# Kernel tuning notes

Measured on AMD Instinct MI355X. Metric: run time of the kernel, lower is better.

The kernel has to match this reference:

```python
import jax, jax.numpy as jnp
import numpy as np

N_USERS = 100000
N_ITEMS = 50000
D = 64
L = 3          # TopKformer_layers
E = 1000000    # number of train (user,item) edges


def setup_inputs() -> dict:
    key = jax.random.key(0)
    k1, k2, k3, k4, k5 = jax.random.split(key, 5)
    return {
        "users_w": jax.random.normal(k1, (N_USERS, D), jnp.float32) * 0.1,
        "items_w": jax.random.normal(k2, (N_ITEMS, D), jnp.float32) * 0.1,
        "beta_w": jax.random.normal(k3, (N_USERS, L), jnp.float32),
        "train_user": jax.random.randint(k4, (E,), 0, N_USERS, dtype=jnp.int32),
        "train_item": jax.random.randint(k5, (E,), 0, N_ITEMS, dtype=jnp.int32),
    }


def reference(users_w, items_w, beta_w, train_user, train_item):
    """Model.computer(): LightGCN-style bipartite propagation where each
    layer's user update is gated by a learned per-user beta = tanh(beta_w).
    Returns concat([user_embs, item_embs]) after L propagation layers."""
    beta = jnp.tanh(beta_w)  # [N_USERS, L], as in Model.beta_value

    # symmetric degree normalization 1/sqrt(d_u * d_i) over train edges
    ones = jnp.ones(train_user.shape[0], users_w.dtype)
    du = jnp.clip(jax.ops.segment_sum(ones, train_user, N_USERS), 1.0)
    di = jnp.clip(jax.ops.segment_sum(ones, train_item, N_ITEMS), 1.0)
    norm = (1.0 / jnp.sqrt(du[train_user] * di[train_item]))[:, None]  # [E,1]

    u_emb, i_emb = users_w, items_w
    for l in range(L):
        # gather neighbor embeddings along edges, scatter-add back (irregular access)
        msg_u = jax.ops.segment_sum(i_emb[train_item] * norm, train_user, N_USERS)
        msg_i = jax.ops.segment_sum(u_emb[train_user] * norm, train_item, N_ITEMS)
        u_emb = msg_u + beta[:, l:l + 1] * u_emb  # beta-weighted residual (per user)
        i_emb = msg_i
    return jnp.concatenate([u_emb, i_emb], axis=0)  # [N_USERS+N_ITEMS, D]
```

## Files before the change

### kernel.cpp

```cpp
#include <hip/hip_runtime.h>

#define NUSERS 100000
#define NITEMS 50000
#define NV (NUSERS + NITEMS)
#define DIM 64
#define NLAYERS 3
#define PAD 64
#define BINSHIFT 9
#define BINSZ 512
#define NBINS ((NV + BINSZ - 1) / BINSZ)
#define EPB 1024

typedef _Float16 half4v __attribute__((ext_vector_type(4)));
typedef _Float16 half8v __attribute__((ext_vector_type(8)));

__global__ void hist_kernel(const int* __restrict__ tu, const int* __restrict__ ti,
                            int* __restrict__ cnt, int E) {
    __shared__ int h[NBINS];
    int t = threadIdx.x, b = blockIdx.x;
    for (int i = t; i < NBINS; i += 256) h[i] = 0;
    __syncthreads();
    int base = b * EPB;
#pragma unroll
    for (int j = 0; j < 4; ++j) {
        int e = base + t + 256 * j;
        if (e < E) {
            atomicAdd(&h[tu[e] >> BINSHIFT], 1);
            atomicAdd(&h[(NUSERS + ti[e]) >> BINSHIFT], 1);
        }
    }
    __syncthreads();
    for (int i = t; i < NBINS; i += 256) cnt[(size_t)b * NBINS + i] = h[i];
}

__global__ void colscan_kernel(int* __restrict__ cnt, int* __restrict__ bintot, int nblk) {
    __shared__ int sh[256];
    int bin = blockIdx.x, t = threadIdx.x;
    int chunk = (nblk + 255) / 256;
    int v[8];
    int sum = 0;
    for (int j = 0; j < chunk; ++j) {
        int blk = t * chunk + j;
        v[j] = (blk < nblk) ? cnt[(size_t)blk * NBINS + bin] : 0;
        sum += v[j];
    }
    sh[t] = sum;
    __syncthreads();
    for (int d = 1; d < 256; d <<= 1) {
        int x = (t >= d) ? sh[t - d] : 0;
        __syncthreads();
        sh[t] += x;
        __syncthreads();
    }
    int run = sh[t] - sum;
    for (int j = 0; j < chunk; ++j) {
        int blk = t * chunk + j;
        if (blk < nblk) { cnt[(size_t)blk * NBINS + bin] = run; run += v[j]; }
    }
    if (t == 255) bintot[bin] = sh[255];
}

__global__ void binscan_kernel(const int* __restrict__ bintot, int* __restrict__ binstart) {
    __shared__ int sh[512];
    int t = threadIdx.x;
    int v = (t < NBINS) ? bintot[t] : 0;
    sh[t] = v;
    __syncthreads();
    for (int d = 1; d < 512; d <<= 1) {
        int x = (t >= d) ? sh[t - d] : 0;
        __syncthreads();
        sh[t] += x;
        __syncthreads();
    }
    if (t < NBINS) binstart[t] = sh[t] - v;
    if (t == NBINS - 1) binstart[NBINS] = sh[t];
}

__global__ void scatter_kernel(const int* __restrict__ tu, const int* __restrict__ ti,
                               const int* __restrict__ cnt, const int* __restrict__ binstart,
                               unsigned int* __restrict__ binbuf, int E) {
    __shared__ int h[NBINS];
    __shared__ int bb[NBINS];
    __shared__ int bs[NBINS];
    int t = threadIdx.x, b = blockIdx.x;
    for (int i = t; i < NBINS; i += 256) {
        h[i] = 0;
        bb[i] = cnt[(size_t)b * NBINS + i];
        bs[i] = binstart[i];
    }
    __syncthreads();
    int base = b * EPB;
#pragma unroll
    for (int j = 0; j < 4; ++j) {
        int e = base + t + 256 * j;
        if (e < E) {
            int u = tu[e];
            int w = NUSERS + ti[e];
            int bu = u >> BINSHIFT, bw = w >> BINSHIFT;
            int r1 = atomicAdd(&h[bu], 1);
            int r2 = atomicAdd(&h[bw], 1);
            binbuf[bs[bu] + bb[bu] + r1] = ((unsigned)(u & (BINSZ - 1)) << 18) | (unsigned)w;
            binbuf[bs[bw] + bb[bw] + r2] = ((unsigned)(w & (BINSZ - 1)) << 18) | (unsigned)u;
        }
    }
}

__global__ void bfill_kernel(const unsigned int* __restrict__ binbuf,
                             const int* __restrict__ binstart,
                             int* __restrict__ deg, int* __restrict__ adj) {
    __shared__ int c[BINSZ];
    int bin = blockIdx.x, t = threadIdx.x;
    c[t] = 0;
    __syncthreads();
    int start = binstart[bin];
    int n = binstart[bin + 1] - start;
    int vbase = bin << BINSHIFT;
    for (int k = t; k < n; k += 512) {
        unsigned rec = binbuf[start + k];
        int vloc = rec >> 18;
        int nbr = (int)(rec & 0x3FFFFu);
        int r = atomicAdd(&c[vloc], 1);
        adj[((vbase + vloc) << 6) + r] = nbr << 7;
    }
    __syncthreads();
    int v = vbase + t;
    if (v < NV) deg[v] = c[t];
}

__global__ void init_kernel(const float* __restrict__ users_w, const float* __restrict__ items_w,
                            const int* __restrict__ deg, _Float16* __restrict__ Yh,
                            _Float16* __restrict__ Dh) {
    int t = blockIdx.x * blockDim.x + threadIdx.x;
    int n4 = NV * (DIM / 4);
    if (t >= n4) {
        int z = t - n4;
        if (z < 16) reinterpret_cast<half4v*>(Yh + (size_t)NV * DIM)[z] = half4v{};
        else if (z < 32) reinterpret_cast<half4v*>(Dh + (size_t)NV * DIM)[z - 16] = half4v{};
        return;
    }
    int v = t >> 4;
    float r = rsqrtf(fmaxf((float)deg[v], 1.0f));
    const float4* src = (v < NUSERS)
        ? reinterpret_cast<const float4*>(users_w) + t
        : reinterpret_cast<const float4*>(items_w) + (t - NUSERS * (DIM / 4));
    float4 x = *src;
    half4v h;
    h.x = (_Float16)(x.x * r);
    h.y = (_Float16)(x.y * r);
    h.z = (_Float16)(x.z * r);
    h.w = (_Float16)(x.w * r);
    reinterpret_cast<half4v*>(Yh)[t] = h;
}

template <bool FINAL>
__global__ void gather_kernel(const _Float16* __restrict__ Yh, const int* __restrict__ deg,
                              const int* __restrict__ adj,
                              const float* __restrict__ beta_w,
                              void* __restrict__ dst_v, int layer) {
    int wid = (blockIdx.x * blockDim.x + threadIdx.x) >> 6;
    int lane = threadIdx.x & 63;
    if (wid >= NV) return;
    int g = lane >> 3;
    int p = lane & 7;
    int s = wid << 6;
    const char* rowb = (const char*)Yh + p * 16;
    const int NVS = NV << 7;

    int dg = deg[wid];
    int raw0 = adj[s + g];
    int raw1 = adj[s + 8 + g];
    int raw2 = adj[s + 16 + g];
    int raw3 = adj[s + 24 + g];
    bool isU = wid < NUSERS;
    float bw_ = 0.f;
    half8v hy = {};
    if (isU && g == 0) {
        bw_ = beta_w[wid * NLAYERS + layer];
        hy = *reinterpret_cast<const half8v*>(Yh + (size_t)wid * DIM + p * 8);
    }

    int o0 = (g      < dg) ? raw0 : NVS;
    int o1 = (8 + g  < dg) ? raw1 : NVS;
    half8v h0 = *reinterpret_cast<const half8v*>(rowb + (size_t)(unsigned)o0);
    half8v h1 = *reinterpret_cast<const half8v*>(rowb + (size_t)(unsigned)o1);

    half8v hs;
    if (dg > 16) {
        int o2 = (16 + g < dg) ? raw2 : NVS;
        int o3 = (24 + g < dg) ? raw3 : NVS;
        half8v h2 = *reinterpret_cast<const half8v*>(rowb + (size_t)(unsigned)o2);
        half8v h3 = *reinterpret_cast<const half8v*>(rowb + (size_t)(unsigned)o3);
        hs = (h0 + h1) + (h2 + h3);
    } else {
        hs = h0 + h1;
    }
    float a[8];
#pragma unroll
    for (int j = 0; j < 8; ++j) a[j] = (float)hs[j];

    if (dg > 32) {
#pragma unroll
        for (int jb = 0; jb < 4; ++jb) {
            int slotbase = 32 + jb * 8;
            if (slotbase < dg) {
                int ks = slotbase + g;
                int rw = adj[s + ks];
                int oj = (ks < dg) ? rw : NVS;
                half8v hj = *reinterpret_cast<const half8v*>(rowb + (size_t)(unsigned)oj);
#pragma unroll
                for (int j = 0; j < 8; ++j) a[j] += (float)hj[j];
            }
        }
    }

#pragma unroll
    for (int j = 0; j < 8; ++j) a[j] += __shfl_xor(a[j], 8);
#pragma unroll
    for (int j = 0; j < 8; ++j) a[j] += __shfl_xor(a[j], 16);
#pragma unroll
    for (int j = 0; j < 8; ++j) a[j] += __shfl_xor(a[j], 32);

    if (g == 0) {
        float fdg = fmaxf((float)dg, 1.0f);
        float r = rsqrtf(fdg);
        float b = isU ? tanhf(bw_) : 0.f;
        if (!FINAL) {
            float rr = r * r;
            half8v o;
#pragma unroll
            for (int j = 0; j < 8; ++j) o[j] = (_Float16)(rr * a[j] + b * (float)hy[j]);
            reinterpret_cast<half8v*>((_Float16*)dst_v + (size_t)wid * DIM)[p] = o;
        } else {
            float c = b * __builtin_sqrtf(fdg);
            float4 o0f, o1f;
            o0f.x = r * a[0] + c * (float)hy[0];
            o0f.y = r * a[1] + c * (float)hy[1];
            o0f.z = r * a[2] + c * (float)hy[2];
            o0f.w = r * a[3] + c * (float)hy[3];
            o1f.x = r * a[4] + c * (float)hy[4];
            o1f.y = r * a[5] + c * (float)hy[5];
            o1f.z = r * a[6] + c * (float)hy[6];
            o1f.w = r * a[7] + c * (float)hy[7];
            float4* dp = reinterpret_cast<float4*>((float*)dst_v + (size_t)wid * DIM + p * 8);
            dp[0] = o0f;
            dp[1] = o1f;
        }
    }
}

extern "C" void kernel_launch(void* const* d_in, const int* in_sizes, int n_in,
                              void* d_out, int out_size, void* d_ws, size_t ws_size,
                              hipStream_t stream) {
    const float* users_w = (const float*)d_in[0];
    const float* items_w = (const float*)d_in[1];
    const float* beta_w  = (const float*)d_in[2];
    const int*   tu      = (const int*)d_in[3];
    const int*   ti      = (const int*)d_in[4];
    const int    E       = in_sizes[3];
    float*       out     = (float*)d_out;

    int nblk = (E + EPB - 1) / EPB;

    char* ws = (char*)d_ws;
    size_t woff = 0;
    auto take = [&](size_t bytes) {
        char* p = ws + woff;
        woff += (bytes + 1023) & ~(size_t)1023;
        return p;
    };
    int*      deg      = (int*)take((size_t)NV * sizeof(int));
    int*      cnt      = (int*)take((size_t)nblk * NBINS * sizeof(int));
    int*      bintot   = (int*)take((size_t)NBINS * sizeof(int));
    int*      binstart = (int*)take((size_t)(NBINS + 1) * sizeof(int));
    unsigned* binbuf   = (unsigned*)take((size_t)2 * E * sizeof(unsigned));
    int*      adj      = (int*)take((size_t)NV * PAD * sizeof(int));
    _Float16* Yh0      = (_Float16*)take((size_t)(NV + 1) * DIM * sizeof(_Float16));

    _Float16* Dh = (_Float16*)d_out;

    const int blk = 256;

    hist_kernel<<<nblk, 256, 0, stream>>>(tu, ti, cnt, E);
    colscan_kernel<<<NBINS, 256, 0, stream>>>(cnt, bintot, nblk);
    binscan_kernel<<<1, 512, 0, stream>>>(bintot, binstart);
    scatter_kernel<<<nblk, 256, 0, stream>>>(tu, ti, cnt, binstart, binbuf, E);
    bfill_kernel<<<NBINS, 512, 0, stream>>>(binbuf, binstart, deg, adj);

    int n4 = NV * (DIM / 4);
    init_kernel<<<(n4 + 32 + blk - 1) / blk, blk, 0, stream>>>(users_w, items_w, deg, Yh0, Dh);

    int gblocks = ((size_t)NV * 64 + blk - 1) / blk;

    gather_kernel<false><<<gblocks, blk, 0, stream>>>(Yh0, deg, adj, beta_w, Dh, 0);
    gather_kernel<false><<<gblocks, blk, 0, stream>>>(Dh, deg, adj, beta_w, Yh0, 1);
    gather_kernel<true ><<<gblocks, blk, 0, stream>>>(Yh0, deg, adj, beta_w, out, 2);
}
```

Baseline: 191.5 us.

## Vectorize edge loads in binning kernels and shortcut low-degree gathers with half shuffles

The histogram and scatter kernels now read four edges per thread with int4 loads and double the edges per block. The scatter kernel also folds the per-bin block offset and bin start into a single shared array. The propagation kernel skips the second neighbor load for vertices of degree 8 or less, and for low-degree vertices does the first cross-lane reduction on packed fp16 pairs, halving that shuffle traffic. This risks fp16 accumulation error and needs E to be 4-aligned for the vector path, with a scalar tail kept as fallback.

```diff
diff --git a/kernel.cpp b/kernel.cpp
--- a/kernel.cpp
+++ b/kernel.cpp
@@ -9,8 +9,9 @@
 #define BINSHIFT 9
 #define BINSZ 512
 #define NBINS ((NV + BINSZ - 1) / BINSZ)
-#define EPB 1024
-
+#define EPB 2048
+
+typedef _Float16 half2v __attribute__((ext_vector_type(2)));
 typedef _Float16 half4v __attribute__((ext_vector_type(4)));
 typedef _Float16 half8v __attribute__((ext_vector_type(8)));
 
@@ -22,11 +23,24 @@
     __syncthreads();
     int base = b * EPB;
 #pragma unroll
-    for (int j = 0; j < 4; ++j) {
-        int e = base + t + 256 * j;
-        if (e < E) {
-            atomicAdd(&h[tu[e] >> BINSHIFT], 1);
-            atomicAdd(&h[(NUSERS + ti[e]) >> BINSHIFT], 1);
+    for (int j = 0; j < 2; ++j) {
+        int e = base + (j * 256 + t) * 4;
+        if (e + 4 <= E) {
+            int4 u4 = *reinterpret_cast<const int4*>(tu + e);
+            int4 i4 = *reinterpret_cast<const int4*>(ti + e);
+            atomicAdd(&h[u4.x >> BINSHIFT], 1);
+            atomicAdd(&h[u4.y >> BINSHIFT], 1);
+            atomicAdd(&h[u4.z >> BINSHIFT], 1);
+            atomicAdd(&h[u4.w >> BINSHIFT], 1);
+            atomicAdd(&h[(NUSERS + i4.x) >> BINSHIFT], 1);
+            atomicAdd(&h[(NUSERS + i4.y) >> BINSHIFT], 1);
+            atomicAdd(&h[(NUSERS + i4.z) >> BINSHIFT], 1);
+            atomicAdd(&h[(NUSERS + i4.w) >> BINSHIFT], 1);
+        } else {
+            for (int k = e; k < E && k < e + 4; ++k) {
+                atomicAdd(&h[tu[k] >> BINSHIFT], 1);
+                atomicAdd(&h[(NUSERS + ti[k]) >> BINSHIFT], 1);
+            }
         }
     }
     __syncthreads();
@@ -80,27 +94,42 @@
                                const int* __restrict__ cnt, const int* __restrict__ binstart,
                                unsigned int* __restrict__ binbuf, int E) {
     __shared__ int h[NBINS];
-    __shared__ int bb[NBINS];
-    __shared__ int bs[NBINS];
+    __shared__ int bbs[NBINS];
     int t = threadIdx.x, b = blockIdx.x;
     for (int i = t; i < NBINS; i += 256) {
         h[i] = 0;
-        bb[i] = cnt[(size_t)b * NBINS + i];
-        bs[i] = binstart[i];
+        bbs[i] = cnt[(size_t)b * NBINS + i] + binstart[i];
     }
     __syncthreads();
     int base = b * EPB;
 #pragma unroll
-    for (int j = 0; j < 4; ++j) {
-        int e = base + t + 256 * j;
-        if (e < E) {
-            int u = tu[e];
-            int w = NUSERS + ti[e];
-            int bu = u >> BINSHIFT, bw = w >> BINSHIFT;
-            int r1 = atomicAdd(&h[bu], 1);
-            int r2 = atomicAdd(&h[bw], 1);
-            binbuf[bs[bu] + bb[bu] + r1] = ((unsigned)(u & (BINSZ - 1)) << 18) | (unsigned)w;
-            binbuf[bs[bw] + bb[bw] + r2] = ((unsigned)(w & (BINSZ - 1)) << 18) | (unsigned)u;
+    for (int j = 0; j < 2; ++j) {
+        int e = base + (j * 256 + t) * 4;
+        if (e + 4 <= E) {
+            int4 u4 = *reinterpret_cast<const int4*>(tu + e);
+            int4 i4 = *reinterpret_cast<const int4*>(ti + e);
+            int us[4] = {u4.x, u4.y, u4.z, u4.w};
+            int is_[4] = {i4.x, i4.y, i4.z, i4.w};
+#pragma unroll
+            for (int k = 0; k < 4; ++k) {
+                int u = us[k];
+                int w = NUSERS + is_[k];
+                int bu = u >> BINSHIFT, bw = w >> BINSHIFT;
+                int r1 = atomicAdd(&h[bu], 1);
+                int r2 = atomicAdd(&h[bw], 1);
+                binbuf[bbs[bu] + r1] = ((unsigned)(u & (BINSZ - 1)) << 18) | (unsigned)w;
+                binbuf[bbs[bw] + r2] = ((unsigned)(w & (BINSZ - 1)) << 18) | (unsigned)u;
+            }
+        } else {
+            for (int k = e; k < E && k < e + 4; ++k) {
+                int u = tu[k];
+                int w = NUSERS + ti[k];
+                int bu = u >> BINSHIFT, bw = w >> BINSHIFT;
+                int r1 = atomicAdd(&h[bu], 1);
+                int r2 = atomicAdd(&h[bw], 1);
+                binbuf[bbs[bu] + r1] = ((unsigned)(u & (BINSZ - 1)) << 18) | (unsigned)w;
+                binbuf[bbs[bw] + r2] = ((unsigned)(w & (BINSZ - 1)) << 18) | (unsigned)u;
+            }
         }
     }
 }
@@ -179,26 +208,20 @@
         hy = *reinterpret_cast<const half8v*>(Yh + (size_t)wid * DIM + p * 8);
     }
 
-    int o0 = (g      < dg) ? raw0 : NVS;
-    int o1 = (8 + g  < dg) ? raw1 : NVS;
+    int o0 = (g < dg) ? raw0 : NVS;
     half8v h0 = *reinterpret_cast<const half8v*>(rowb + (size_t)(unsigned)o0);
-    half8v h1 = *reinterpret_cast<const half8v*>(rowb + (size_t)(unsigned)o1);
-
-    half8v hs;
-    if (dg > 16) {
+
+    float a[8];
+    if (dg > 32) {
+        int o1 = (8 + g  < dg) ? raw1 : NVS;
         int o2 = (16 + g < dg) ? raw2 : NVS;
         int o3 = (24 + g < dg) ? raw3 : NVS;
+        half8v h1 = *reinterpret_cast<const half8v*>(rowb + (size_t)(unsigned)o1);
         half8v h2 = *reinterpret_cast<const half8v*>(rowb + (size_t)(unsigned)o2);
         half8v h3 = *reinterpret_cast<const half8v*>(rowb + (size_t)(unsigned)o3);
-        hs = (h0 + h1) + (h2 + h3);
-    } else {
-        hs = h0 + h1;
-    }
-    float a[8];
-#pragma unroll
-    for (int j = 0; j < 8; ++j) a[j] = (float)hs[j];
-
-    if (dg > 32) {
+        half8v hs = (h0 + h1) + (h2 + h3);
+#pragma unroll
+        for (int j = 0; j < 8; ++j) a[j] = (float)hs[j];
 #pragma unroll
         for (int jb = 0; jb < 4; ++jb) {
             int slotbase = 32 + jb * 8;
@@ -211,10 +234,39 @@
                 for (int j = 0; j < 8; ++j) a[j] += (float)hj[j];
             }
         }
-    }
-
-#pragma unroll
-    for (int j = 0; j < 8; ++j) a[j] += __shfl_xor(a[j], 8);
+#pragma unroll
+        for (int j = 0; j < 8; ++j) a[j] += __shfl_xor(a[j], 8);
+    } else {
+        half8v hsum;
+        if (dg > 16) {
+            int o1 = (8 + g  < dg) ? raw1 : NVS;
+            int o2 = (16 + g < dg) ? raw2 : NVS;
+            int o3 = (24 + g < dg) ? raw3 : NVS;
+            half8v h1 = *reinterpret_cast<const half8v*>(rowb + (size_t)(unsigned)o1);
+            half8v h2 = *reinterpret_cast<const half8v*>(rowb + (size_t)(unsigned)o2);
+            half8v h3 = *reinterpret_cast<const half8v*>(rowb + (size_t)(unsigned)o3);
+            hsum = (h0 + h1) + (h2 + h3);
+        } else if (dg > 8) {
+            int o1 = (8 + g < dg) ? raw1 : NVS;
+            half8v h1 = *reinterpret_cast<const half8v*>(rowb + (size_t)(unsigned)o1);
+            hsum = h0 + h1;
+        } else {
+            hsum = h0;
+        }
+        union { half8v h; int i[4]; } u;
+        u.h = hsum;
+#pragma unroll
+        for (int j = 0; j < 4; ++j) {
+            int o = __shfl_xor(u.i[j], 8);
+            half2v x = __builtin_bit_cast(half2v, u.i[j]);
+            half2v y = __builtin_bit_cast(half2v, o);
+            x = x + y;
+            u.i[j] = __builtin_bit_cast(int, x);
+        }
+#pragma unroll
+        for (int j = 0; j < 8; ++j) a[j] = (float)u.h[j];
+    }
+
 #pragma unroll
     for (int j = 0; j < 8; ++j) a[j] += __shfl_xor(a[j], 16);
 #pragma unroll
```

Result: faster. 182.3 us (median of 2 runs) (-4.8%).
